# Kernel optimization log

Measured on AMD Instinct MI355X. Metric: run time of the kernel, lower is better.

## Reference

```python
import jax, jax.numpy as jnp
import numpy as np

EPS = 1e-5

def _ln(x, g, b):
    m = jnp.mean(x, axis=-1, keepdims=True)
    v = jnp.var(x, axis=-1, keepdims=True)
    return (x - m) * jax.lax.rsqrt(v + EPS) * g + b

def _gelu(x):
    return jax.nn.gelu(x, approximate=False)  # torch nn.GELU default is exact erf

def setup_inputs() -> dict:
    key = jax.random.key(0)
    B, N, D, H = 4, 1024, 128, 12
    HID = H * D
    ks = jax.random.split(key, 16)
    s = lambda k, sh, fan: jax.random.normal(k, sh, jnp.float32) * (fan ** -0.5)
    return {
        "x": jax.random.normal(ks[0], (B, N, D), jnp.float32),
        # project: LN(D) -> Linear(D,HID) -> GELU -> Linear(HID,HID)
        "ln1_g": jnp.ones((D,), jnp.float32), "ln1_b": jnp.zeros((D,), jnp.float32),
        "W1": s(ks[1], (D, HID), D), "b1": jnp.zeros((HID,), jnp.float32),
        "W2": s(ks[2], (HID, HID), HID), "b2": jnp.zeros((HID,), jnp.float32),
        # shared Attention(inc=D, outc=D)
        "aln_g": jnp.ones((D,), jnp.float32), "aln_b": jnp.zeros((D,), jnp.float32),
        "Wqkv": s(ks[3], (D, 3 * D), D), "bqkv": jnp.zeros((3 * D,), jnp.float32),
        "Wl": s(ks[4], (D, D), D), "bl": jnp.zeros((D,), jnp.float32),
        # out_proj: LN(HID) -> Linear(HID, D) -> GELU
        "lno_g": jnp.ones((HID,), jnp.float32), "lno_b": jnp.zeros((HID,), jnp.float32),
        "Wo": s(ks[5], (HID, D), HID), "bo": jnp.zeros((D,), jnp.float32),
    }

def reference(x, ln1_g, ln1_b, W1, b1, W2, b2,
              aln_g, aln_b, Wqkv, bqkv, Wl, bl,
              lno_g, lno_b, Wo, bo):
    B, N, D = x.shape
    # project (dropout is identity in eval mode)
    h = _ln(x, ln1_g, ln1_b)
    h = _gelu(h @ W1 + b1)
    h = h @ W2 + b2                      # [B, N, H*D]
    H = h.shape[-1] // D
    # chunk along last dim into H features of width D; fold heads into batch
    f = h.reshape(B, N, H, D).transpose(0, 2, 1, 3).reshape(B * H, N, D)
    # shared Attention applied to each head-chunk
    a = _ln(f, aln_g, aln_b)
    qkv = a @ Wqkv + bqkv
    q, k, v = jnp.split(qkv, 3, axis=-1)
    scores = jax.nn.softmax(jnp.einsum('bnd,bmd->bnm', q, k) * (D ** -0.5), axis=-1)
    o = jnp.einsum('bnm,bmd->bnd', scores, v)
    o = o @ Wl + bl
    o = _gelu(o + f)                     # [B*H, N, D]
    # concat heads back along last dim
    feats = o.reshape(B, H, N, D).transpose(0, 2, 1, 3).reshape(B, N, H * D)
    out = _gelu(_ln(feats, lno_g, lno_b) @ Wo + bo)
    return out
```

## Files before the change

kernel.cpp:

```cpp
#include <hip/hip_runtime.h>
#include <stdint.h>

typedef unsigned short u16;
typedef __attribute__((ext_vector_type(8))) short short8;
typedef __attribute__((ext_vector_type(4))) float floatx4;

__device__ inline float b2f(u16 u) {
  union { uint32_t i; float f; } x; x.i = ((uint32_t)u) << 16; return x.f;
}
__device__ inline u16 f2b(float f) {
  union { float f; uint32_t i; } x; x.f = f;
  uint32_t r = (x.i + 0x7FFFu + ((x.i >> 16) & 1u)) >> 16;
  return (u16)r;
}
__device__ inline float gelu_f(float v) {
  return 0.5f * v * (1.0f + erff(v * 0.70710678118654752440f));
}

#define MFMA16(a, b, c) __builtin_amdgcn_mfma_f32_16x16x32_bf16((a), (b), (c), 0, 0, 0)

__device__ __forceinline__ void gl2lds16(const u16* g, u16* l) {
  __builtin_amdgcn_global_load_lds(
      (const __attribute__((address_space(1))) uint32_t*)(uintptr_t)g,
      (__attribute__((address_space(3))) uint32_t*)(uint32_t)(uintptr_t)l,
      16, 0, 0);
}

__global__ __launch_bounds__(256)
void tpose_all_kernel(const float* __restrict__ W1, const float* __restrict__ W2,
                      const float* __restrict__ Wqkv, const float* __restrict__ Wl,
                      const float* __restrict__ Wo,
                      u16* __restrict__ w1t, u16* __restrict__ w2t,
                      u16* __restrict__ wqkvt, u16* __restrict__ wlt,
                      u16* __restrict__ wot) {
  int id = blockIdx.x;
  const float* src; u16* dst; int R, C, bx, by;
  if (id < 2304)      { src = W2;   dst = w2t;   R = 1536; C = 1536; bx = (id % 48) * 32; by = (id / 48) * 32; }
  else if (id < 2496) { id -= 2304; src = W1;   dst = w1t;   R = 128;  C = 1536; bx = (id % 48) * 32; by = (id / 48) * 32; }
  else if (id < 2688) { id -= 2496; src = Wo;   dst = wot;   R = 1536; C = 128;  bx = (id % 4) * 32;  by = (id / 4) * 32; }
  else if (id < 2736) { id -= 2688; src = Wqkv; dst = wqkvt; R = 128;  C = 384;  bx = (id % 12) * 32; by = (id / 12) * 32; }
  else                { id -= 2736; src = Wl;   dst = wlt;   R = 128;  C = 128;  bx = (id % 4) * 32;  by = (id / 4) * 32; }
  __shared__ u16 t[32][33];
  int tx = threadIdx.x & 31, ty = threadIdx.x >> 5;
  for (int i = 0; i < 32; i += 8)
    t[ty + i][tx] = f2b(src[(size_t)(by + ty + i) * C + bx + tx]);
  __syncthreads();
  for (int i = 0; i < 32; i += 8)
    dst[(size_t)(bx + ty + i) * R + by + tx] = t[tx][ty + i];
}

__global__ __launch_bounds__(256)
void ln128_f32_kernel(const float* __restrict__ X, const float* __restrict__ g,
                      const float* __restrict__ bb, u16* __restrict__ Y) {
  int tid = threadIdx.x, w = tid >> 6, lane = tid & 63;
  int row = blockIdx.x * 4 + w;
  const float* xr = X + (size_t)row * 128;
  float2 xv = *(const float2*)(xr + lane * 2);
  float x0 = xv.x, x1 = xv.y;
  float s = x0 + x1, s2 = x0 * x0 + x1 * x1;
  for (int m = 1; m < 64; m <<= 1) { s += __shfl_xor(s, m, 64); s2 += __shfl_xor(s2, m, 64); }
  float mean = s * (1.0f / 128.0f);
  float var = s2 * (1.0f / 128.0f) - mean * mean;
  float rstd = 1.0f / sqrtf(var + 1e-5f);
  float2 gv = *(const float2*)(g + lane * 2);
  float2 bv = *(const float2*)(bb + lane * 2);
  float y0 = (x0 - mean) * rstd * gv.x + bv.x;
  float y1 = (x1 - mean) * rstd * gv.y + bv.y;
  *(uint32_t*)(Y + (size_t)row * 128 + lane * 2) =
      (uint32_t)f2b(y0) | ((uint32_t)f2b(y1) << 16);
}

__global__ __launch_bounds__(256)
void ln128_perm_kernel(const u16* __restrict__ X, const float* __restrict__ g,
                       const float* __restrict__ bb, u16* __restrict__ Y) {
  int tid = threadIdx.x, w = tid >> 6, lane = tid & 63;
  int rid = blockIdx.x * 4 + w;
  int bh = rid >> 10, n = rid & 1023;
  int b = bh / 12, h = bh % 12;
  const u16* xr = X + ((size_t)(b * 1024 + n)) * 1536 + h * 128;
  uint32_t u = *(const uint32_t*)(xr + lane * 2);
  float x0 = b2f(u & 0xffff), x1 = b2f(u >> 16);
  float s = x0 + x1, s2 = x0 * x0 + x1 * x1;
  for (int m = 1; m < 64; m <<= 1) { s += __shfl_xor(s, m, 64); s2 += __shfl_xor(s2, m, 64); }
  float mean = s * (1.0f / 128.0f);
  float var = s2 * (1.0f / 128.0f) - mean * mean;
  float rstd = 1.0f / sqrtf(var + 1e-5f);
  float2 gv = *(const float2*)(g + lane * 2);
  float2 bv = *(const float2*)(bb + lane * 2);
  float y0 = (x0 - mean) * rstd * gv.x + bv.x;
  float y1 = (x1 - mean) * rstd * gv.y + bv.y;
  *(uint32_t*)(Y + (size_t)rid * 128 + lane * 2) =
      (uint32_t)f2b(y0) | ((uint32_t)f2b(y1) << 16);
}

__global__ __launch_bounds__(256)
void ln1536_kernel(const u16* __restrict__ X, const float* __restrict__ g,
                   const float* __restrict__ bb, u16* __restrict__ Y) {
  int row = blockIdx.x, tid = threadIdx.x;
  const u16* xr = X + (size_t)row * 1536;
  uint32_t u0 = *(const uint32_t*)(xr + tid * 6);
  uint32_t u1 = *(const uint32_t*)(xr + tid * 6 + 2);
  uint32_t u2 = *(const uint32_t*)(xr + tid * 6 + 4);
  float v[6] = { b2f(u0 & 0xffff), b2f(u0 >> 16), b2f(u1 & 0xffff),
                 b2f(u1 >> 16),    b2f(u2 & 0xffff), b2f(u2 >> 16) };
  float s = 0.f, s2 = 0.f;
  for (int j = 0; j < 6; j++) { s += v[j]; s2 += v[j] * v[j]; }
  for (int m = 1; m < 64; m <<= 1) { s += __shfl_xor(s, m, 64); s2 += __shfl_xor(s2, m, 64); }
  __shared__ float red[8];
  int w = tid >> 6, lane = tid & 63;
  if (lane == 0) { red[w] = s; red[4 + w] = s2; }
  __syncthreads();
  s = red[0] + red[1] + red[2] + red[3];
  s2 = red[4] + red[5] + red[6] + red[7];
  float mean = s * (1.0f / 1536.0f);
  float var = s2 * (1.0f / 1536.0f) - mean * mean;
  float rstd = 1.0f / sqrtf(var + 1e-5f);
  uint32_t o[3];
  for (int p = 0; p < 3; p++) {
    int c = tid * 6 + p * 2;
    float y0 = (v[p * 2] - mean) * rstd * g[c] + bb[c];
    float y1 = (v[p * 2 + 1] - mean) * rstd * g[c + 1] + bb[c + 1];
    o[p] = (uint32_t)f2b(y0) | ((uint32_t)f2b(y1) << 16);
  }
  u16* yr = Y + (size_t)row * 1536 + tid * 6;
  *(uint32_t*)(yr) = o[0];
  *(uint32_t*)(yr + 2) = o[1];
  *(uint32_t*)(yr + 4) = o[2];
}

__global__ __launch_bounds__(256)
void qkv_kernel(const u16* __restrict__ A, const u16* __restrict__ BT,
                const float* __restrict__ bias, u16* __restrict__ qkv,
                u16* __restrict__ vT) {
  const int K = 128;
  __shared__ __align__(16) u16 abuf[128 * 32];
  __shared__ __align__(16) u16 bbuf[128 * 32];
  int tid = threadIdx.x;
  int w = tid >> 6, lane = tid & 63, ln = lane & 15, quad = lane >> 4;
  int bm = blockIdx.x * 128, bn = blockIdx.y * 128;
  int wr = w >> 1, wc = w & 1;
  floatx4 acc[4][4] = {};
  for (int k0 = 0; k0 < K; k0 += 32) {
    __syncthreads();
    for (int rd = 0; rd < 2; rd++) {
      int c = tid + rd * 256;
      int row = c >> 2, col = (c & 3) * 8;
      gl2lds16(A + (size_t)(bm + row) * K + k0 + col, abuf + c * 8);
      gl2lds16(BT + (size_t)(bn + row) * K + k0 + col, bbuf + c * 8);
    }
    __syncthreads();
    short8 af[4], bf[4];
    for (int i = 0; i < 4; i++)
      af[i] = *(const short8*)(abuf + (wr * 64 + i * 16 + ln) * 32 + quad * 8);
    for (int j = 0; j < 4; j++)
      bf[j] = *(const short8*)(bbuf + (wc * 64 + j * 16 + ln) * 32 + quad * 8);
    for (int i = 0; i < 4; i++)
      for (int j = 0; j < 4; j++)
        acc[i][j] = MFMA16(af[i], bf[j], acc[i][j]);
  }
  if (blockIdx.y < 2) {
    for (int i = 0; i < 4; i++) {
      int row0 = bm + wr * 64 + i * 16 + quad * 4;
      for (int j = 0; j < 4; j++) {
        int col = bn + wc * 64 + j * 16 + ln;
        float bv = bias[col];
        for (int r = 0; r < 4; r++)
          qkv[(size_t)(row0 + r) * 256 + col] = f2b(acc[i][j][r] + bv);
      }
    }
  } else {
    int bh = bm >> 10;
    int nb = bm & 1023;
    u16* vp = vT + (size_t)bh * 128 * 1024;
    for (int i = 0; i < 4; i++) {
      int n0 = nb + wr * 64 + i * 16 + quad * 4;
      int npos = (n0 & ~31) | (((n0 >> 2) & 3) * 8) | (((n0 >> 4) & 1) * 4);
      for (int j = 0; j < 4; j++) {
        int d = wc * 64 + j * 16 + ln;
        float bv = bias[256 + d];
        u16 tmp[4];
        for (int r = 0; r < 4; r++) tmp[r] = f2b(acc[i][j][r] + bv);
        *(uint2*)(vp + (size_t)d * 1024 + npos) = *(const uint2*)tmp;
      }
    }
  }
}

template <int GELU, int RES, typename OUTT>
__global__ __launch_bounds__(256)
void gemm64_kernel(const u16* __restrict__ A, const u16* __restrict__ BT,
                   const float* __restrict__ bias, const u16* __restrict__ res,
                   OUTT* __restrict__ C, int M, int N, int K) {
  __shared__ __align__(16) u16 abuf[64 * 32];
  __shared__ __align__(16) u16 bbuf[128 * 32];
  int tid = threadIdx.x;
  int w = tid >> 6, lane = tid & 63, ln = lane & 15, quad = lane >> 4;
  int bm = blockIdx.x * 64, bn = blockIdx.y * 128;
  floatx4 acc[4][2] = {};
  for (int k0 = 0; k0 < K; k0 += 32) {
    __syncthreads();
    for (int rd = 0; rd < 2; rd++) {
      int c = tid + rd * 256;
      int row = c >> 2, col = (c & 3) * 8;
      gl2lds16(BT + (size_t)(bn + row) * K + k0 + col, bbuf + c * 8);
    }
    {
      int c = tid;
      int row = c >> 2, col = (c & 3) * 8;
      gl2lds16(A + (size_t)(bm + row) * K + k0 + col, abuf + c * 8);
    }
    __syncthreads();
    short8 af[4], bf[2];
    for (int i = 0; i < 4; i++)
      af[i] = *(const short8*)(abuf + (i * 16 + ln) * 32 + quad * 8);
    for (int j = 0; j < 2; j++)
      bf[j] = *(const short8*)(bbuf + (w * 32 + j * 16 + ln) * 32 + quad * 8);
    for (int i = 0; i < 4; i++)
      for (int j = 0; j < 2; j++)
        acc[i][j] = MFMA16(af[i], bf[j], acc[i][j]);
  }
  for (int i = 0; i < 4; i++) {
    int row0 = bm + i * 16 + quad * 4;
    for (int j = 0; j < 2; j++) {
      int col = bn + w * 32 + j * 16 + ln;
      float bv = bias[col];
      for (int r = 0; r < 4; r++) {
        float v = acc[i][j][r] + bv;
        if (RES) v += b2f(res[(size_t)(row0 + r) * N + col]);
        if (GELU) v = gelu_f(v);
        if constexpr (sizeof(OUTT) == 2)
          C[(size_t)(row0 + r) * N + col] = f2b(v);
        else
          C[(size_t)(row0 + r) * N + col] = v;
      }
    }
  }
}

template <int GELU, int RES, typename OUTT>
__global__ __launch_bounds__(256)
void gemm64b_kernel(const u16* __restrict__ A, const u16* __restrict__ BT,
                    const float* __restrict__ bias, const u16* __restrict__ res,
                    OUTT* __restrict__ C, int M, int N, int K) {
  __shared__ __align__(16) u16 abuf[2 * 64 * 32];
  __shared__ __align__(16) u16 bbuf[2 * 128 * 32];
  int tid = threadIdx.x;
  int w = tid >> 6, lane = tid & 63, ln = lane & 15, quad = lane >> 4;
  int bm = blockIdx.x * 64, bn = blockIdx.y * 128;
  floatx4 acc[4][2] = {};
  for (int k0 = 0; k0 < K; k0 += 64) {
    __syncthreads();
    for (int ks = 0; ks < 2; ks++) {
      {
        int c = tid;
        int row = c >> 2, cc = c & 3;
        gl2lds16(A + (size_t)(bm + row) * K + k0 + ks * 32 + cc * 8,
                 abuf + ks * 2048 + c * 8);
      }
      for (int rd = 0; rd < 2; rd++) {
        int c = tid + rd * 256;
        int row = c >> 2, cc = c & 3;
        gl2lds16(BT + (size_t)(bn + row) * K + k0 + ks * 32 + cc * 8,
                 bbuf + ks * 4096 + c * 8);
      }
    }
    __syncthreads();
    short8 af[2][4], bf[2][2];
    for (int ks = 0; ks < 2; ks++) {
      for (int i = 0; i < 4; i++)
        af[ks][i] = *(const short8*)(abuf + ks * 2048 + (i * 16 + ln) * 32 + quad * 8);
      for (int j = 0; j < 2; j++)
        bf[ks][j] = *(const short8*)(bbuf + ks * 4096 + (w * 32 + j * 16 + ln) * 32 + quad * 8);
    }
    for (int i = 0; i < 4; i++)
      for (int j = 0; j < 2; j++) {
        acc[i][j] = MFMA16(af[0][i], bf[0][j], acc[i][j]);
        acc[i][j] = MFMA16(af[1][i], bf[1][j], acc[i][j]);
      }
  }
  for (int i = 0; i < 4; i++) {
    int row0 = bm + i * 16 + quad * 4;
    for (int j = 0; j < 2; j++) {
      int col = bn + w * 32 + j * 16 + ln;
      float bv = bias[col];
      for (int r = 0; r < 4; r++) {
        float v = acc[i][j][r] + bv;
        if (RES) v += b2f(res[(size_t)(row0 + r) * N + col]);
        if (GELU) v = gelu_f(v);
        if constexpr (sizeof(OUTT) == 2)
          C[(size_t)(row0 + r) * N + col] = f2b(v);
        else
          C[(size_t)(row0 + r) * N + col] = v;
      }
    }
  }
}

__global__ __launch_bounds__(256)
void gemmwl_kernel(const u16* __restrict__ A, const u16* __restrict__ BT,
                   const float* __restrict__ bias, const u16* __restrict__ res,
                   u16* __restrict__ feats) {
  const int K = 128;
  __shared__ __align__(16) u16 abuf[64 * 32];
  __shared__ __align__(16) u16 bbuf[128 * 32];
  int tid = threadIdx.x;
  int w = tid >> 6, lane = tid & 63, ln = lane & 15, quad = lane >> 4;
  int bm = blockIdx.x * 64;
  floatx4 acc[4][2] = {};
  for (int k0 = 0; k0 < K; k0 += 32) {
    __syncthreads();
    for (int rd = 0; rd < 2; rd++) {
      int c = tid + rd * 256;
      int row = c >> 2, col = (c & 3) * 8;
      gl2lds16(BT + (size_t)row * K + k0 + col, bbuf + c * 8);
    }
    {
      int c = tid;
      int row = c >> 2, col = (c & 3) * 8;
      gl2lds16(A + (size_t)(bm + row) * K + k0 + col, abuf + c * 8);
    }
    __syncthreads();
    short8 af[4], bf[2];
    for (int i = 0; i < 4; i++)
      af[i] = *(const short8*)(abuf + (i * 16 + ln) * 32 + quad * 8);
    for (int j = 0; j < 2; j++)
      bf[j] = *(const short8*)(bbuf + (w * 32 + j * 16 + ln) * 32 + quad * 8);
    for (int i = 0; i < 4; i++)
      for (int j = 0; j < 2; j++)
        acc[i][j] = MFMA16(af[i], bf[j], acc[i][j]);
  }
  int bh = bm >> 10, nb = bm & 1023;
  int b = bh / 12, hh = bh % 12;
  size_t obase = ((size_t)b * 1024) * 1536 + hh * 128;
  for (int i = 0; i < 4; i++) {
    int n0 = nb + i * 16 + quad * 4;
    for (int j = 0; j < 2; j++) {
      int col = w * 32 + j * 16 + ln;
      float bv = bias[col];
      for (int r = 0; r < 4; r++) {
        size_t idx = obase + (size_t)(n0 + r) * 1536 + col;
        float v = acc[i][j][r] + bv + b2f(res[idx]);
        feats[idx] = f2b(gelu_f(v));
      }
    }
  }
}

__global__ __launch_bounds__(256)
void gemm64_part_kernel(const u16* __restrict__ A, const u16* __restrict__ BT,
                        float* __restrict__ pws, int Kfull, int kspan) {
  __shared__ __align__(16) u16 abuf[64 * 32];
  __shared__ __align__(16) u16 bbuf[128 * 32];
  int tid = threadIdx.x;
  int w = tid >> 6, lane = tid & 63, ln = lane & 15, quad = lane >> 4;
  int bm = blockIdx.x * 64;
  int kbeg = blockIdx.y * kspan, kend = kbeg + kspan;
  float* Cp = pws + (size_t)blockIdx.y * 4096 * 128;
  floatx4 acc[4][2] = {};
  for (int k0 = kbeg; k0 < kend; k0 += 32) {
    __syncthreads();
    for (int rd = 0; rd < 2; rd++) {
      int c = tid + rd * 256;
      int row = c >> 2, col = (c & 3) * 8;
      gl2lds16(BT + (size_t)row * Kfull + k0 + col, bbuf + c * 8);
    }
    {
      int c = tid;
      int row = c >> 2, col = (c & 3) * 8;
      gl2lds16(A + (size_t)(bm + row) * Kfull + k0 + col, abuf + c * 8);
    }
    __syncthreads();
    short8 af[4], bf[2];
    for (int i = 0; i < 4; i++)
      af[i] = *(const short8*)(abuf + (i * 16 + ln) * 32 + quad * 8);
    for (int j = 0; j < 2; j++)
      bf[j] = *(const short8*)(bbuf + (w * 32 + j * 16 + ln) * 32 + quad * 8);
    for (int i = 0; i < 4; i++)
      for (int j = 0; j < 2; j++)
        acc[i][j] = MFMA16(af[i], bf[j], acc[i][j]);
  }
  for (int i = 0; i < 4; i++) {
    int row0 = bm + i * 16 + quad * 4;
    for (int j = 0; j < 2; j++) {
      int col = w * 32 + j * 16 + ln;
      for (int r = 0; r < 4; r++)
        Cp[(size_t)(row0 + r) * 128 + col] = acc[i][j][r];
    }
  }
}

__global__ __launch_bounds__(256)
void combine_wo_kernel(const float* __restrict__ p, const float* __restrict__ bias,
                       float* __restrict__ out) {
  int i = blockIdx.x * 256 + threadIdx.x;
  const int SZ = 4096 * 128;
  float v = p[i] + p[i + SZ] + p[i + 2 * SZ] + p[i + 3 * SZ] + bias[i & 127];
  out[i] = gelu_f(v);
}

__global__ __launch_bounds__(256, 3)
void attn_kernel(const u16* __restrict__ qkv, const u16* __restrict__ vT,
                 u16* __restrict__ obuf) {
  int blk = blockIdx.x;
  int xcd = blk & 7, slot = blk >> 3;
  int bh = xcd * 6 + (slot >> 4);
  int qt = slot & 15;
  int tid = threadIdx.x, w = tid >> 6, lane = tid & 63, ln = lane & 15, quad = lane >> 4;
  int pair = w & 1, half = w >> 1;
  __shared__ __align__(16) u16 smem[24576 + 128];
  u16* kbuf = smem;
  u16* vbufs = smem + 8192;
  const int rs = 256;
  size_t base = (size_t)bh * 1024 * 256;
  const u16* qp = qkv + base;
  const u16* kp = qkv + base + 128;
  const u16* vp = vT + (size_t)bh * 128 * 1024;

  short8 qf[2][4];
  for (int g = 0; g < 2; g++) {
    int qrow = qt * 64 + pair * 32 + g * 16 + ln;
    for (int st = 0; st < 4; st++)
      qf[g][st] = *(const short8*)(qp + (size_t)qrow * rs + st * 32 + quad * 8);
  }

  floatx4 o[2][8] = {};
  float lsum[2] = {0.f, 0.f};
  const float K2 = 0.08838834764831845f * 1.4426950408889634f;

  auto STAGE_K = [&](int kt) {
    for (int it = 0; it < 4; it++) {
      int c = it * 256 + tid;
      int st = c >> 8, key = (c >> 2) & 63, cc = c & 3;
      gl2lds16(kp + (size_t)(kt * 64 + key) * rs + st * 32 + cc * 8, kbuf + c * 8);
    }
  };
  auto STAGE_V = [&](int kt, int buf) {
    u16* vb = vbufs + buf * 8192;
    for (int it = 0; it < 4; it++) {
      int c = it * 256 + tid;
      int kf = c >> 9, d = (c >> 2) & 127, cc = c & 3;
      gl2lds16(vp + (size_t)d * 1024 + kt * 64 + kf * 32 + cc * 8, vb + c * 8);
    }
  };

  STAGE_K(0);
  STAGE_V(0, 0);

  for (int kt = 0; kt < 16; kt++) {
    __syncthreads();

    short8 kfr[2][4];
    for (int tt = 0; tt < 2; tt++)
      for (int st = 0; st < 4; st++)
        kfr[tt][st] = *(const short8*)(kbuf + st * 2048 +
                                       ((half * 2 + tt) * 16 + ln) * 32 + quad * 8);
    __syncthreads();

    if (kt < 15) {
      STAGE_K(kt + 1);
      STAGE_V(kt + 1, (kt + 1) & 1);
    }

    floatx4 s[2][2] = {};
    for (int tt = 0; tt < 2; tt++)
      for (int st = 0; st < 4; st++) {
        s[0][tt] = MFMA16(kfr[tt][st], qf[0][st], s[0][tt]);
        s[1][tt] = MFMA16(kfr[tt][st], qf[1][st], s[1][tt]);
      }

    short8 pfrag[2];
    for (int g = 0; g < 2; g++) {
      float p0[4], p1[4];
      for (int r = 0; r < 4; r++) {
        p0[r] = exp2f(s[g][0][r] * K2);
        p1[r] = exp2f(s[g][1][r] * K2);
        lsum[g] += p0[r] + p1[r];
      }
      uint32_t a0, a1, b0, b1;
      asm("v_cvt_pk_bf16_f32 %0, %1, %2" : "=v"(a0) : "v"(p0[0]), "v"(p0[1]));
      asm("v_cvt_pk_bf16_f32 %0, %1, %2" : "=v"(a1) : "v"(p0[2]), "v"(p0[3]));
      asm("v_cvt_pk_bf16_f32 %0, %1, %2" : "=v"(b0) : "v"(p1[0]), "v"(p1[1]));
      asm("v_cvt_pk_bf16_f32 %0, %1, %2" : "=v"(b1) : "v"(p1[2]), "v"(p1[3]));
      union { uint32_t u[4]; short8 v; } pu;
      pu.u[0] = a0; pu.u[1] = a1; pu.u[2] = b0; pu.u[3] = b1;
      pfrag[g] = pu.v;
    }

    const u16* vb = vbufs + (kt & 1) * 8192;
    for (int dt = 0; dt < 8; dt++) {
      short8 av = *(const short8*)(vb + half * 4096 + (dt * 16 + ln) * 32 + quad * 8);
      o[0][dt] = MFMA16(av, pfrag[0], o[0][dt]);
      o[1][dt] = MFMA16(av, pfrag[1], o[1][dt]);
    }
  }

  for (int g = 0; g < 2; g++) {
    lsum[g] += __shfl_xor(lsum[g], 16, 64);
    lsum[g] += __shfl_xor(lsum[g], 32, 64);
  }

  __syncthreads();
  float* mbuf = (float*)smem;
  float* lbuf = (float*)(smem + 16384);
  if (half == 1) {
    float* mp = mbuf + pair * 4096;
    for (int g = 0; g < 2; g++)
      for (int dt = 0; dt < 8; dt++)
        for (int r = 0; r < 4; r++)
          mp[(dt * 16 + quad * 4 + r) * 32 + ((g * 16 + ln + quad * 8) & 31)] = o[g][dt][r];
    if (quad == 0) {
      lbuf[pair * 32 + ln] = lsum[0];
      lbuf[pair * 32 + 16 + ln] = lsum[1];
    }
  }
  __syncthreads();
  if (half == 0) {
    float* mp = mbuf + pair * 4096;
    for (int g = 0; g < 2; g++) {
      float lt = lsum[g] + lbuf[pair * 32 + g * 16 + ln];
      float inv = 1.0f / lt;
      int n = qt * 64 + pair * 32 + g * 16 + ln;
      size_t ob = ((size_t)bh * 1024 + n) * 128;
      for (int dt = 0; dt < 8; dt++) {
        u16 tmp[4];
        for (int r = 0; r < 4; r++)
          tmp[r] = f2b((o[g][dt][r] +
                        mp[(dt * 16 + quad * 4 + r) * 32 + ((g * 16 + ln + quad * 8) & 31)]) * inv);
        *(uint2*)(obuf + ob + dt * 16 + quad * 4) = *(const uint2*)tmp;
      }
    }
  }
}

extern "C" void kernel_launch(void* const* d_in, const int* in_sizes, int n_in,
                              void* d_out, int out_size, void* d_ws, size_t ws_size,
                              hipStream_t stream) {
  (void)in_sizes; (void)n_in; (void)out_size; (void)ws_size;
  const float* x    = (const float*)d_in[0];
  const float* ln1g = (const float*)d_in[1];
  const float* ln1b = (const float*)d_in[2];
  const float* W1   = (const float*)d_in[3];
  const float* b1   = (const float*)d_in[4];
  const float* W2   = (const float*)d_in[5];
  const float* b2   = (const float*)d_in[6];
  const float* alng = (const float*)d_in[7];
  const float* alnb = (const float*)d_in[8];
  const float* Wqkv = (const float*)d_in[9];
  const float* bqkv = (const float*)d_in[10];
  const float* Wl   = (const float*)d_in[11];
  const float* bl   = (const float*)d_in[12];
  const float* lnog = (const float*)d_in[13];
  const float* lnob = (const float*)d_in[14];
  const float* Wo   = (const float*)d_in[15];
  const float* bo   = (const float*)d_in[16];
  float* out = (float*)d_out;

  char* ws = (char*)d_ws;
  size_t off = 0;
  auto alloc = [&](size_t elems) { u16* p = (u16*)(ws + off); off += elems * sizeof(u16); return p; };
  u16* w1t   = alloc((size_t)1536 * 128);
  u16* w2t   = alloc((size_t)1536 * 1536);
  u16* wqkvt = alloc((size_t)384 * 128);
  u16* wlt   = alloc((size_t)128 * 128);
  u16* wot   = alloc((size_t)128 * 1536);
  u16* lnx   = alloc((size_t)4096 * 128);
  u16* h1    = alloc((size_t)4096 * 1536);
  u16* h2    = alloc((size_t)4096 * 1536);
  u16* aln   = alloc((size_t)49152 * 128);
  u16* qkv   = alloc((size_t)49152 * 256);
  u16* obuf  = alloc((size_t)49152 * 128);
  u16* vT = h1;
  u16* feats = aln;
  u16* lnf = qkv;
  float* pws = (float*)h1;

  dim3 T(256);
  tpose_all_kernel<<<dim3(2752), T, 0, stream>>>(W1, W2, Wqkv, Wl, Wo,
                                                 w1t, w2t, wqkvt, wlt, wot);
  ln128_f32_kernel<<<dim3(4096 / 4), T, 0, stream>>>(x, ln1g, ln1b, lnx);
  gemm64_kernel<1, 0, u16><<<dim3(4096 / 64, 1536 / 128), T, 0, stream>>>(
      lnx, w1t, b1, nullptr, h1, 4096, 1536, 128);
  gemm64b_kernel<0, 0, u16><<<dim3(4096 / 64, 1536 / 128), T, 0, stream>>>(
      h1, w2t, b2, nullptr, h2, 4096, 1536, 1536);
  ln128_perm_kernel<<<dim3(49152 / 4), T, 0, stream>>>(h2, alng, alnb, aln);
  qkv_kernel<<<dim3(49152 / 128, 3), T, 0, stream>>>(aln, wqkvt, bqkv, qkv, vT);
  attn_kernel<<<dim3(768), T, 0, stream>>>(qkv, vT, obuf);
  gemmwl_kernel<<<dim3(49152 / 64), T, 0, stream>>>(obuf, wlt, bl, h2, feats);
  ln1536_kernel<<<dim3(4096), T, 0, stream>>>(feats, lnog, lnob, lnf);
  gemm64_part_kernel<<<dim3(4096 / 64, 4), T, 0, stream>>>(lnf, wot, pws, 1536, 384);
  combine_wo_kernel<<<dim3(4096 * 128 / 256), T, 0, stream>>>(pws, bo, out);
}
```

Measured before the change: 241.6 us.

## Use double-buffered 128x128 GEMMs, prescale Q, and compute softmax row sums via MFMA

Replaces the 64x128 GEMM kernels for the two project-MLP matmuls with a 128x128 tile kernel that double-buffers LDS staging, so more output is reused per loaded tile and loads overlap compute. The softmax scale and log2e factor are folded into Q when the QKV kernel writes it, removing a multiply per score in attention. Attention row sums are now accumulated with an extra MFMA against a ones fragment instead of per-lane adds and shuffles. Tradeoffs: the larger tile halves the block count for the 4096-row GEMMs, and Q rounded to bf16 after scaling changes numerics slightly.

Result: slower. 282.9 us (+17.1%).

```diff
diff --git a/kernel.cpp b/kernel.cpp
--- a/kernel.cpp
+++ b/kernel.cpp
@@ -159,13 +159,15 @@
         acc[i][j] = MFMA16(af[i], bf[j], acc[i][j]);
   }
   if (blockIdx.y < 2) {
+    const float QSCALE = 0.08838834764831845f * 1.4426950408889634f;
+    float scale = (blockIdx.y == 0) ? QSCALE : 1.0f;
     for (int i = 0; i < 4; i++) {
       int row0 = bm + wr * 64 + i * 16 + quad * 4;
       for (int j = 0; j < 4; j++) {
         int col = bn + wc * 64 + j * 16 + ln;
         float bv = bias[col];
         for (int r = 0; r < 4; r++)
-          qkv[(size_t)(row0 + r) * 256 + col] = f2b(acc[i][j][r] + bv);
+          qkv[(size_t)(row0 + r) * 256 + col] = f2b((acc[i][j][r] + bv) * scale);
       }
     }
   } else {
@@ -186,111 +188,53 @@
   }
 }
 
-template <int GELU, int RES, typename OUTT>
-__global__ __launch_bounds__(256)
-void gemm64_kernel(const u16* __restrict__ A, const u16* __restrict__ BT,
-                   const float* __restrict__ bias, const u16* __restrict__ res,
-                   OUTT* __restrict__ C, int M, int N, int K) {
-  __shared__ __align__(16) u16 abuf[64 * 32];
-  __shared__ __align__(16) u16 bbuf[128 * 32];
+template <int GELU>
+__global__ __launch_bounds__(256)
+void gemm128_kernel(const u16* __restrict__ A, const u16* __restrict__ BT,
+                    const float* __restrict__ bias, u16* __restrict__ C,
+                    int M, int N, int K) {
+  __shared__ __align__(16) u16 abuf[2 * 128 * 32];
+  __shared__ __align__(16) u16 bbuf[2 * 128 * 32];
   int tid = threadIdx.x;
   int w = tid >> 6, lane = tid & 63, ln = lane & 15, quad = lane >> 4;
-  int bm = blockIdx.x * 64, bn = blockIdx.y * 128;
-  floatx4 acc[4][2] = {};
-  for (int k0 = 0; k0 < K; k0 += 32) {
-    __syncthreads();
+  int bm = blockIdx.x * 128, bn = blockIdx.y * 128;
+  int wr = w >> 1, wc = w & 1;
+  floatx4 acc[4][4] = {};
+  auto STAGE = [&](int k0, int buf) {
+    u16* ab = abuf + buf * 4096;
+    u16* bb = bbuf + buf * 4096;
     for (int rd = 0; rd < 2; rd++) {
       int c = tid + rd * 256;
       int row = c >> 2, col = (c & 3) * 8;
-      gl2lds16(BT + (size_t)(bn + row) * K + k0 + col, bbuf + c * 8);
-    }
-    {
-      int c = tid;
-      int row = c >> 2, col = (c & 3) * 8;
-      gl2lds16(A + (size_t)(bm + row) * K + k0 + col, abuf + c * 8);
-    }
-    __syncthreads();
-    short8 af[4], bf[2];
-    for (int i = 0; i < 4; i++)
-      af[i] = *(const short8*)(abuf + (i * 16 + ln) * 32 + quad * 8);
-    for (int j = 0; j < 2; j++)
-      bf[j] = *(const short8*)(bbuf + (w * 32 + j * 16 + ln) * 32 + quad * 8);
-    for (int i = 0; i < 4; i++)
-      for (int j = 0; j < 2; j++)
+      gl2lds16(A + (size_t)(bm + row) * K + k0 + col, ab + c * 8);
+      gl2lds16(BT + (size_t)(bn + row) * K + k0 + col, bb + c * 8);
+    }
+  };
+  STAGE(0, 0);
+  int it = 0;
+  for (int k0 = 0; k0 < K; k0 += 32, it++) {
+    __syncthreads();
+    if (k0 + 32 < K) STAGE(k0 + 32, (it + 1) & 1);
+    const u16* ab = abuf + (it & 1) * 4096;
+    const u16* bb = bbuf + (it & 1) * 4096;
+    short8 af[4], bf[4];
+    for (int i = 0; i < 4; i++)
+      af[i] = *(const short8*)(ab + (wr * 64 + i * 16 + ln) * 32 + quad * 8);
+    for (int j = 0; j < 4; j++)
+      bf[j] = *(const short8*)(bb + (wc * 64 + j * 16 + ln) * 32 + quad * 8);
+    for (int i = 0; i < 4; i++)
+      for (int j = 0; j < 4; j++)
         acc[i][j] = MFMA16(af[i], bf[j], acc[i][j]);
   }
   for (int i = 0; i < 4; i++) {
-    int row0 = bm + i * 16 + quad * 4;
-    for (int j = 0; j < 2; j++) {
-      int col = bn + w * 32 + j * 16 + ln;
+    int row0 = bm + wr * 64 + i * 16 + quad * 4;
+    for (int j = 0; j < 4; j++) {
+      int col = bn + wc * 64 + j * 16 + ln;
       float bv = bias[col];
       for (int r = 0; r < 4; r++) {
         float v = acc[i][j][r] + bv;
-        if (RES) v += b2f(res[(size_t)(row0 + r) * N + col]);
         if (GELU) v = gelu_f(v);
-        if constexpr (sizeof(OUTT) == 2)
-          C[(size_t)(row0 + r) * N + col] = f2b(v);
-        else
-          C[(size_t)(row0 + r) * N + col] = v;
-      }
-    }
-  }
-}
-
-template <int GELU, int RES, typename OUTT>
-__global__ __launch_bounds__(256)
-void gemm64b_kernel(const u16* __restrict__ A, const u16* __restrict__ BT,
-                    const float* __restrict__ bias, const u16* __restrict__ res,
-                    OUTT* __restrict__ C, int M, int N, int K) {
-  __shared__ __align__(16) u16 abuf[2 * 64 * 32];
-  __shared__ __align__(16) u16 bbuf[2 * 128 * 32];
-  int tid = threadIdx.x;
-  int w = tid >> 6, lane = tid & 63, ln = lane & 15, quad = lane >> 4;
-  int bm = blockIdx.x * 64, bn = blockIdx.y * 128;
-  floatx4 acc[4][2] = {};
-  for (int k0 = 0; k0 < K; k0 += 64) {
-    __syncthreads();
-    for (int ks = 0; ks < 2; ks++) {
-      {
-        int c = tid;
-        int row = c >> 2, cc = c & 3;
-        gl2lds16(A + (size_t)(bm + row) * K + k0 + ks * 32 + cc * 8,
-                 abuf + ks * 2048 + c * 8);
-      }
-      for (int rd = 0; rd < 2; rd++) {
-        int c = tid + rd * 256;
-        int row = c >> 2, cc = c & 3;
-        gl2lds16(BT + (size_t)(bn + row) * K + k0 + ks * 32 + cc * 8,
-                 bbuf + ks * 4096 + c * 8);
-      }
-    }
-    __syncthreads();
-    short8 af[2][4], bf[2][2];
-    for (int ks = 0; ks < 2; ks++) {
-      for (int i = 0; i < 4; i++)
-        af[ks][i] = *(const short8*)(abuf + ks * 2048 + (i * 16 + ln) * 32 + quad * 8);
-      for (int j = 0; j < 2; j++)
-        bf[ks][j] = *(const short8*)(bbuf + ks * 4096 + (w * 32 + j * 16 + ln) * 32 + quad * 8);
-    }
-    for (int i = 0; i < 4; i++)
-      for (int j = 0; j < 2; j++) {
-        acc[i][j] = MFMA16(af[0][i], bf[0][j], acc[i][j]);
-        acc[i][j] = MFMA16(af[1][i], bf[1][j], acc[i][j]);
-      }
-  }
-  for (int i = 0; i < 4; i++) {
-    int row0 = bm + i * 16 + quad * 4;
-    for (int j = 0; j < 2; j++) {
-      int col = bn + w * 32 + j * 16 + ln;
-      float bv = bias[col];
-      for (int r = 0; r < 4; r++) {
-        float v = acc[i][j][r] + bv;
-        if (RES) v += b2f(res[(size_t)(row0 + r) * N + col]);
-        if (GELU) v = gelu_f(v);
-        if constexpr (sizeof(OUTT) == 2)
-          C[(size_t)(row0 + r) * N + col] = f2b(v);
-        else
-          C[(size_t)(row0 + r) * N + col] = v;
+        C[(size_t)(row0 + r) * N + col] = f2b(v);
       }
     }
   }
@@ -423,9 +367,14 @@
       qf[g][st] = *(const short8*)(qp + (size_t)qrow * rs + st * 32 + quad * 8);
   }
 
+  short8 onesA;
+  {
+    short v = (ln == 0) ? (short)0x3F80 : (short)0;
+    for (int j = 0; j < 8; j++) onesA[j] = v;
+  }
+
   floatx4 o[2][8] = {};
-  float lsum[2] = {0.f, 0.f};
-  const float K2 = 0.08838834764831845f * 1.4426950408889634f;
+  floatx4 l9[2] = {};
 
   auto STAGE_K = [&](int kt) {
     for (int it = 0; it < 4; it++) {
@@ -472,9 +421,8 @@
     for (int g = 0; g < 2; g++) {
       float p0[4], p1[4];
       for (int r = 0; r < 4; r++) {
-        p0[r] = exp2f(s[g][0][r] * K2);
-        p1[r] = exp2f(s[g][1][r] * K2);
-        lsum[g] += p0[r] + p1[r];
+        p0[r] = exp2f(s[g][0][r]);
+        p1[r] = exp2f(s[g][1][r]);
       }
       uint32_t a0, a1, b0, b1;
       asm("v_cvt_pk_bf16_f32 %0, %1, %2" : "=v"(a0) : "v"(p0[0]), "v"(p0[1]));
@@ -486,6 +434,9 @@
       pfrag[g] = pu.v;
     }
 
+    l9[0] = MFMA16(onesA, pfrag[0], l9[0]);
+    l9[1] = MFMA16(onesA, pfrag[1], l9[1]);
+
     const u16* vb = vbufs + (kt & 1) * 8192;
     for (int dt = 0; dt < 8; dt++) {
       short8 av = *(const short8*)(vb + half * 4096 + (dt * 16 + ln) * 32 + quad * 8);
@@ -494,10 +445,9 @@
     }
   }
 
-  for (int g = 0; g < 2; g++) {
-    lsum[g] += __shfl_xor(lsum[g], 16, 64);
-    lsum[g] += __shfl_xor(lsum[g], 32, 64);
-  }
+  float lsum[2];
+  lsum[0] = __shfl(l9[0][0], ln);
+  lsum[1] = __shfl(l9[1][0], ln);
 
   __syncthreads();
   float* mbuf = (float*)smem;
@@ -578,10 +528,10 @@
   tpose_all_kernel<<<dim3(2752), T, 0, stream>>>(W1, W2, Wqkv, Wl, Wo,
                                                  w1t, w2t, wqkvt, wlt, wot);
   ln128_f32_kernel<<<dim3(4096 / 4), T, 0, stream>>>(x, ln1g, ln1b, lnx);
-  gemm64_kernel<1, 0, u16><<<dim3(4096 / 64, 1536 / 128), T, 0, stream>>>(
-      lnx, w1t, b1, nullptr, h1, 4096, 1536, 128);
-  gemm64b_kernel<0, 0, u16><<<dim3(4096 / 64, 1536 / 128), T, 0, stream>>>(
-      h1, w2t, b2, nullptr, h2, 4096, 1536, 1536);
+  gemm128_kernel<1><<<dim3(4096 / 128, 1536 / 128), T, 0, stream>>>(
+      lnx, w1t, b1, h1, 4096, 1536, 128);
+  gemm128_kernel<0><<<dim3(4096 / 128, 1536 / 128), T, 0, stream>>>(
+      h1, w2t, b2, h2, 4096, 1536, 1536);
   ln128_perm_kernel<<<dim3(49152 / 4), T, 0, stream>>>(h2, alng, alnb, aln);
   qkv_kernel<<<dim3(49152 / 128, 3), T, 0, stream>>>(aln, wqkvt, bqkv, qkv, vT);
   attn_kernel<<<dim3(768), T, 0, stream>>>(qkv, vT, obuf);
```
